# Performance work log

Hardware: AMD Instinct MI355X
Metric: run time of the kernel (lower is better)

## Reference

```python
import jax, jax.numpy as jnp
import numpy as np

DIM = 256
NUM_HEADS = 8
HEAD_DIM = DIM // NUM_HEADS
KERNEL_SIZES = (5, 7, 9)
DILATIONS = (1, 2, 3)
HEADS_PER_RANGE = (4, 3, 1)  # replicates torch allocation: weights~1/k^2, floor + greedy remainder
SCALE = HEAD_DIM ** -0.5


def _unfold(x, ks, dil):
    # x: (B, h, d, H, W) -> (B, h, d, L, H, W), L = ks*ks, same-padded dilated neighborhood gather
    B, h, d, H, W = x.shape
    pad = (ks // 2) * dil
    xp = jnp.pad(x, ((0, 0), (0, 0), (0, 0), (pad, pad), (pad, pad)))
    patches = [xp[..., i * dil:i * dil + H, j * dil:j * dil + W]
               for i in range(ks) for j in range(ks)]
    return jnp.stack(patches, axis=3)


def _attend_range(q, k, v, ks, dil, rpb):
    # q,k,v: (B, h_i, d, H, W); rpb: (h_i, L)
    k_nb = _unfold(k, ks, dil)  # (B,h,d,L,H,W)
    v_nb = _unfold(v, ks, dil)
    logits = jnp.einsum('bhdxy,bhdlxy->bhlxy', q * SCALE, k_nb)
    logits = logits + rpb[None, :, :, None, None]
    attn = jax.nn.softmax(logits, axis=2)
    return jnp.einsum('bhlxy,bhdlxy->bhdxy', attn, v_nb)


def setup_inputs() -> dict:
    key = jax.random.key(0)
    ks = jax.random.split(key, 6)
    B, C, H, W = 4, DIM, 64, 64
    s = 0.02
    inp = {
        'x': jax.random.normal(ks[0], (B, C, H, W), dtype=jnp.float32),
        'qkv_w': jax.random.normal(ks[1], (3 * DIM, DIM), dtype=jnp.float32) * s,
        'qkv_b': jnp.zeros((3 * DIM,), dtype=jnp.float32),
        'proj_w': jax.random.normal(ks[2], (DIM, DIM), dtype=jnp.float32) * s,
        'proj_b': jnp.zeros((DIM,), dtype=jnp.float32),
    }
    for i, kk in enumerate(KERNEL_SIZES):
        inp[f'rpb{i}'] = jax.random.normal(ks[3 + i], (HEADS_PER_RANGE[i], kk * kk), dtype=jnp.float32) * s
    return inp


def reference(x, qkv_w, qkv_b, proj_w, proj_b, rpb0, rpb1, rpb2):
    B, C, H, W = x.shape
    qkv = jnp.einsum('oc,bcxy->boxy', qkv_w, x) + qkv_b[None, :, None, None]
    q, k, v = jnp.split(qkv, 3, axis=1)
    q = q.reshape(B, NUM_HEADS, HEAD_DIM, H, W)
    k = k.reshape(B, NUM_HEADS, HEAD_DIM, H, W)
    v = v.reshape(B, NUM_HEADS, HEAD_DIM, H, W)
    rpbs = (rpb0, rpb1, rpb2)
    outs = []
    hs = 0
    for i in range(len(KERNEL_SIZES)):
        he = hs + HEADS_PER_RANGE[i]
        outs.append(_attend_range(q[:, hs:he], k[:, hs:he], v[:, hs:he],
                                  KERNEL_SIZES[i], DILATIONS[i], rpbs[i]))
        hs = he
    out = jnp.concatenate(outs, axis=1).reshape(B, C, H, W)
    out = jnp.einsum('oc,bcxy->boxy', proj_w, out) + proj_b[None, :, None, None]
    return out
```

## Files before the change

kernel.cpp:

```cpp
#include <hip/hip_runtime.h>
#include <math.h>

#define H_IMG 64
#define W_IMG 64
#define PIX   (H_IMG * W_IMG)
#define NB    4
#define NHEADS 8
#define HD    32
#define CDIM  256
#define QKV_C 768
#define ATT_SCALE 0.17677669529663687f

typedef _Float16 half8_t __attribute__((ext_vector_type(8)));
typedef _Float16 half2_t __attribute__((ext_vector_type(2)));
typedef float f32x4 __attribute__((ext_vector_type(4)));

__global__ void cvt_f16(const float* __restrict__ src, _Float16* __restrict__ dst, int n) {
    int i = blockIdx.x * 256 + threadIdx.x;
    if (i < n) dst[i] = (_Float16)src[i];
}

__launch_bounds__(256)
__global__ void transpose_to_f16(const float* __restrict__ src,
                                 _Float16* __restrict__ dst, int C) {
    __shared__ _Float16 tl[64][66];
    const int b  = blockIdx.z;
    const int p0 = blockIdx.x * 64;
    const int c0 = blockIdx.y * 64;
    const int tx = threadIdx.x;
    const int ty = threadIdx.y;
    const float* s = src + (size_t)b * C * PIX;
    _Float16* d = dst + (size_t)b * PIX * C;
#pragma unroll
    for (int cc = ty; cc < 64; cc += 4)
        tl[cc][tx] = (_Float16)s[(size_t)(c0 + cc) * PIX + p0 + tx];
    __syncthreads();
#pragma unroll
    for (int pp = ty; pp < 64; pp += 4)
        d[(size_t)(p0 + pp) * C + c0 + tx] = tl[tx][pp];
}

template <typename OutT, bool PAIR>
__launch_bounds__(256)
__global__ void gemm16(const _Float16* __restrict__ A,
                       const _Float16* __restrict__ BT,
                       const float* __restrict__ bias,
                       OutT* __restrict__ Y,
                       int M, int K, int N) {
    __shared__ _Float16 Asl[128][40];
    __shared__ _Float16 Bsl[128][40];
    const int b = blockIdx.z;
    const _Float16* Bb = BT + (size_t)b * N * K;
    OutT* Yb = Y + (size_t)b * M * N;
    const int m0 = blockIdx.y * 128;
    const int n0 = blockIdx.x * 128;
    const int t    = threadIdx.x;
    const int lane = t & 63;
    const int w    = t >> 6;
    const int wm = w >> 1, wn = w & 1;
    const int l15 = lane & 15;
    const int kq  = (lane >> 4) * 8;

    f32x4 acc[4][4];
#pragma unroll
    for (int mt = 0; mt < 4; mt++)
#pragma unroll
        for (int nt = 0; nt < 4; nt++)
            acc[mt][nt] = (f32x4){0.f, 0.f, 0.f, 0.f};

    for (int k0 = 0; k0 < K; k0 += 32) {
        __syncthreads();
#pragma unroll
        for (int i = 0; i < 2; i++) {
            int idx = t + i * 256;
            int row = idx >> 2;
            int seg = (idx & 3) * 8;
            *(half8_t*)&Asl[row][seg] = *(const half8_t*)(A  + (size_t)(m0 + row) * K + k0 + seg);
            *(half8_t*)&Bsl[row][seg] = *(const half8_t*)(Bb + (size_t)(n0 + row) * K + k0 + seg);
        }
        __syncthreads();
        half8_t af[4], bf[4];
#pragma unroll
        for (int mt = 0; mt < 4; mt++)
            af[mt] = *(const half8_t*)&Asl[wm * 64 + mt * 16 + l15][kq];
#pragma unroll
        for (int nt = 0; nt < 4; nt++)
            bf[nt] = *(const half8_t*)&Bsl[wn * 64 + nt * 16 + l15][kq];
#pragma unroll
        for (int mt = 0; mt < 4; mt++)
#pragma unroll
            for (int nt = 0; nt < 4; nt++)
                acc[mt][nt] = __builtin_amdgcn_mfma_f32_16x16x32_f16(
                    af[mt], bf[nt], acc[mt][nt], 0, 0, 0);
    }

    const int rq = lane >> 4;
    if constexpr (PAIR) {
        unsigned* Yp = (unsigned*)Yb;
#pragma unroll
        for (int mt = 0; mt < 4; mt++) {
#pragma unroll
            for (int s = 0; s < 2; s++) {
                int mp = m0 + wm * 64 + mt * 16 + rq * 4 + 2 * s;
                float b0 = bias[mp], b1 = bias[mp + 1];
#pragma unroll
                for (int nt = 0; nt < 4; nt++) {
                    int col = n0 + wn * 64 + nt * 16 + l15;
                    half2_t hv;
                    hv.x = (_Float16)(acc[mt][nt][2 * s]     + b0);
                    hv.y = (_Float16)(acc[mt][nt][2 * s + 1] + b1);
                    Yp[(size_t)(mp >> 1) * N + col] = __builtin_bit_cast(unsigned, hv);
                }
            }
        }
    } else {
#pragma unroll
        for (int mt = 0; mt < 4; mt++) {
#pragma unroll
            for (int r = 0; r < 4; r++) {
                int m = m0 + wm * 64 + mt * 16 + rq * 4 + r;
                float bs = bias[m];
                OutT* yp = Yb + (size_t)m * N + n0 + wn * 64;
#pragma unroll
                for (int nt = 0; nt < 4; nt++)
                    yp[nt * 16 + l15] = (OutT)(acc[mt][nt][r] + bs);
            }
        }
    }
}

template <int KS, int DIL>
__device__ __forceinline__ void attn_wave(const unsigned* __restrict__ base,
                                          const float* __restrict__ rp,
                                          float* __restrict__ outp,
                                          int h, int y) {
    const int x = threadIdx.x;

    const unsigned* qb = base + (size_t)(h * 16) * PIX + y * W_IMG + x;
    const unsigned* kb = base + (size_t)(128 + h * 16) * PIX + x;
    const unsigned* vb = base + (size_t)(256 + h * 16) * PIX + x;

    half2_t qh[16];
#pragma unroll
    for (int d2 = 0; d2 < 16; d2++)
        qh[d2] = __builtin_bit_cast(half2_t, qb[(size_t)d2 * PIX]);

    float acc[HD];
#pragma unroll
    for (int d = 0; d < HD; d++) acc[d] = 0.f;
    float denom = 0.f;

#pragma unroll 1
    for (int i = 0; i < KS; i++) {
        const int yy = y + (i - KS / 2) * DIL;
        const float* rrow = rp + i * KS;
        if ((unsigned)yy < (unsigned)H_IMG) {
            int kr[16], vr[16];
            const unsigned* ko = kb + yy * W_IMG;
            const unsigned* vo = vb + yy * W_IMG;
#pragma unroll
            for (int d2 = 0; d2 < 16; d2++) {
                kr[d2] = (int)ko[(size_t)d2 * PIX];
                vr[d2] = (int)vo[(size_t)d2 * PIX];
            }
#pragma unroll
            for (int j = 0; j < KS; j++) {
                const int xx = x + (j - KS / 2) * DIL;
                const int src = xx & 63;
                const bool vx = (unsigned)xx < (unsigned)W_IMG;
                float s = 0.f;
#pragma unroll
                for (int d2 = 0; d2 < 16; d2++) {
                    half2_t kk = __builtin_bit_cast(half2_t, __shfl(kr[d2], src));
#if __has_builtin(__builtin_amdgcn_fdot2)
                    s = __builtin_amdgcn_fdot2(qh[d2], kk, s, false);
#else
                    s += (float)qh[d2].x * (float)kk.x + (float)qh[d2].y * (float)kk.y;
#endif
                }
                const float rb = rrow[j];
                float logit = fmaf(s, ATT_SCALE, rb);
                logit = vx ? logit : rb;
                const float wgt = __expf(logit);
                denom += wgt;
                const float wv = vx ? wgt : 0.f;
#pragma unroll
                for (int d2 = 0; d2 < 16; d2++) {
                    half2_t vv = __builtin_bit_cast(half2_t, __shfl(vr[d2], src));
                    acc[2 * d2]     += wv * (float)vv.x;
                    acc[2 * d2 + 1] += wv * (float)vv.y;
                }
            }
        } else {
#pragma unroll
            for (int j = 0; j < KS; j++) denom += __expf(rrow[j]);
        }
    }

    const float inv = 1.f / denom;
#pragma unroll
    for (int d = 0; d < HD; d++) outp[(size_t)d * PIX] = acc[d] * inv;
}

__launch_bounds__(256)
__global__ void attn_v3(const unsigned* __restrict__ qkv,
                        const float* __restrict__ rpb0,
                        const float* __restrict__ rpb1,
                        const float* __restrict__ rpb2,
                        float* __restrict__ out) {
    const int b  = blockIdx.x >> 1;
    const int hh = blockIdx.x & 1;
    const int y  = blockIdx.y;
    const int ty = threadIdx.y;
    const int h = hh ? (3 + ty) : ((ty == 3) ? 7 : ty);

    const unsigned* base = qkv + (size_t)b * (QKV_C / 2) * PIX;
    float* outp = out + ((size_t)b * CDIM + h * HD) * PIX + y * W_IMG + threadIdx.x;

    if (h < 4) {
        attn_wave<5, 1>(base, rpb0 + h * 25, outp, h, y);
    } else if (h < 7) {
        attn_wave<7, 2>(base, rpb1 + (h - 4) * 49, outp, h, y);
    } else {
        attn_wave<9, 3>(base, rpb2, outp, h, y);
    }
}

extern "C" void kernel_launch(void* const* d_in, const int* in_sizes, int n_in,
                              void* d_out, int out_size, void* d_ws, size_t ws_size,
                              hipStream_t stream) {
    const float* x      = (const float*)d_in[0];
    const float* qkv_w  = (const float*)d_in[1];
    const float* qkv_b  = (const float*)d_in[2];
    const float* proj_w = (const float*)d_in[3];
    const float* proj_b = (const float*)d_in[4];
    const float* rpb0   = (const float*)d_in[5];
    const float* rpb1   = (const float*)d_in[6];
    const float* rpb2   = (const float*)d_in[7];
    float* out = (float*)d_out;

    char* ws = (char*)d_ws;
    _Float16* qkv16 = (_Float16*)ws;
    float*    att32 = (float*)(ws + (size_t)NB * QKV_C * PIX * 2);
    _Float16* T16   = (_Float16*)(ws + (size_t)NB * QKV_C * PIX * 2 + (size_t)NB * CDIM * PIX * 4);
    _Float16* W16   = T16 + (size_t)NB * PIX * CDIM;
    _Float16* P16   = W16 + (size_t)QKV_C * CDIM;

    cvt_f16<<<dim3((QKV_C * CDIM + 255) / 256), dim3(256), 0, stream>>>(qkv_w, W16, QKV_C * CDIM);
    cvt_f16<<<dim3((CDIM * CDIM + 255) / 256), dim3(256), 0, stream>>>(proj_w, P16, CDIM * CDIM);

    transpose_to_f16<<<dim3(PIX / 64, CDIM / 64, NB), dim3(64, 4), 0, stream>>>(x, T16, CDIM);

    gemm16<_Float16, true><<<dim3(PIX / 128, QKV_C / 128, NB), dim3(256), 0, stream>>>(
        W16, T16, qkv_b, qkv16, QKV_C, CDIM, PIX);

    attn_v3<<<dim3(NB * 2, H_IMG), dim3(64, 4), 0, stream>>>(
        (const unsigned*)qkv16, rpb0, rpb1, rpb2, att32);

    transpose_to_f16<<<dim3(PIX / 64, CDIM / 64, NB), dim3(64, 4), 0, stream>>>(att32, T16, CDIM);

    gemm16<float, false><<<dim3(PIX / 128, CDIM / 128, NB), dim3(256), 0, stream>>>(
        P16, T16, proj_b, out, CDIM, CDIM, PIX);
}
```

Before: 171.3 us.

## Fuse attention output transpose into attention kernel and merge weight conversions

The attention kernel now writes fp16 output directly in pixel-major (transposed) layout with 16-byte vector stores. This removes the separate fp32 att buffer and its transpose_to_f16 pass. Blocks are remapped so each block handles one head over four rows, which gives uniform kernel sizes per block instead of mixing heads. The QK dot product is split into four independent accumulators for ILP, and the two weight-conversion launches are merged into one. The strided per-pixel 64-byte stores and rounding the attention output to fp16 before projection are possible costs.

```diff
diff --git a/kernel.cpp b/kernel.cpp
--- a/kernel.cpp
+++ b/kernel.cpp
@@ -15,9 +15,12 @@
 typedef _Float16 half2_t __attribute__((ext_vector_type(2)));
 typedef float f32x4 __attribute__((ext_vector_type(4)));
 
-__global__ void cvt_f16(const float* __restrict__ src, _Float16* __restrict__ dst, int n) {
+__global__ void cvt_w16(const float* __restrict__ a, int na,
+                        const float* __restrict__ b, int nb,
+                        _Float16* __restrict__ da, _Float16* __restrict__ db) {
     int i = blockIdx.x * 256 + threadIdx.x;
-    if (i < n) dst[i] = (_Float16)src[i];
+    if (i < na) da[i] = (_Float16)a[i];
+    else if (i - na < nb) db[i - na] = (_Float16)b[i - na];
 }
 
 __launch_bounds__(256)
@@ -132,7 +135,7 @@
 template <int KS, int DIL>
 __device__ __forceinline__ void attn_wave(const unsigned* __restrict__ base,
                                           const float* __restrict__ rp,
-                                          float* __restrict__ outp,
+                                          _Float16* __restrict__ outp,
                                           int h, int y) {
     const int x = threadIdx.x;
 
@@ -168,18 +171,27 @@
                 const int xx = x + (j - KS / 2) * DIL;
                 const int src = xx & 63;
                 const bool vx = (unsigned)xx < (unsigned)W_IMG;
-                float s = 0.f;
-#pragma unroll
-                for (int d2 = 0; d2 < 16; d2++) {
-                    half2_t kk = __builtin_bit_cast(half2_t, __shfl(kr[d2], src));
+                float s0 = 0.f, s1 = 0.f, s2 = 0.f, s3 = 0.f;
+#pragma unroll
+                for (int d2 = 0; d2 < 16; d2 += 4) {
+                    half2_t k0 = __builtin_bit_cast(half2_t, __shfl(kr[d2 + 0], src));
+                    half2_t k1 = __builtin_bit_cast(half2_t, __shfl(kr[d2 + 1], src));
+                    half2_t k2 = __builtin_bit_cast(half2_t, __shfl(kr[d2 + 2], src));
+                    half2_t k3 = __builtin_bit_cast(half2_t, __shfl(kr[d2 + 3], src));
 #if __has_builtin(__builtin_amdgcn_fdot2)
-                    s = __builtin_amdgcn_fdot2(qh[d2], kk, s, false);
+                    s0 = __builtin_amdgcn_fdot2(qh[d2 + 0], k0, s0, false);
+                    s1 = __builtin_amdgcn_fdot2(qh[d2 + 1], k1, s1, false);
+                    s2 = __builtin_amdgcn_fdot2(qh[d2 + 2], k2, s2, false);
+                    s3 = __builtin_amdgcn_fdot2(qh[d2 + 3], k3, s3, false);
 #else
-                    s += (float)qh[d2].x * (float)kk.x + (float)qh[d2].y * (float)kk.y;
+                    s0 += (float)qh[d2+0].x * (float)k0.x + (float)qh[d2+0].y * (float)k0.y;
+                    s1 += (float)qh[d2+1].x * (float)k1.x + (float)qh[d2+1].y * (float)k1.y;
+                    s2 += (float)qh[d2+2].x * (float)k2.x + (float)qh[d2+2].y * (float)k2.y;
+                    s3 += (float)qh[d2+3].x * (float)k3.x + (float)qh[d2+3].y * (float)k3.y;
 #endif
                 }
                 const float rb = rrow[j];
-                float logit = fmaf(s, ATT_SCALE, rb);
+                float logit = fmaf((s0 + s1) + (s2 + s3), ATT_SCALE, rb);
                 logit = vx ? logit : rb;
                 const float wgt = __expf(logit);
                 denom += wgt;
@@ -199,23 +211,27 @@
 
     const float inv = 1.f / denom;
 #pragma unroll
-    for (int d = 0; d < HD; d++) outp[(size_t)d * PIX] = acc[d] * inv;
+    for (int g = 0; g < 4; g++) {
+        half8_t hv;
+#pragma unroll
+        for (int e = 0; e < 8; e++) hv[e] = (_Float16)(acc[g * 8 + e] * inv);
+        *(half8_t*)(outp + g * 8) = hv;
+    }
 }
 
 __launch_bounds__(256)
-__global__ void attn_v3(const unsigned* __restrict__ qkv,
+__global__ void attn_v4(const unsigned* __restrict__ qkv,
                         const float* __restrict__ rpb0,
                         const float* __restrict__ rpb1,
                         const float* __restrict__ rpb2,
-                        float* __restrict__ out) {
-    const int b  = blockIdx.x >> 1;
-    const int hh = blockIdx.x & 1;
-    const int y  = blockIdx.y;
-    const int ty = threadIdx.y;
-    const int h = hh ? (3 + ty) : ((ty == 3) ? 7 : ty);
+                        _Float16* __restrict__ outT) {
+    const int b = blockIdx.x >> 3;
+    const int h = blockIdx.x & 7;
+    const int y = blockIdx.y * 4 + threadIdx.y;
 
     const unsigned* base = qkv + (size_t)b * (QKV_C / 2) * PIX;
-    float* outp = out + ((size_t)b * CDIM + h * HD) * PIX + y * W_IMG + threadIdx.x;
+    const int p = y * W_IMG + threadIdx.x;
+    _Float16* outp = outT + ((size_t)b * PIX + p) * CDIM + h * HD;
 
     if (h < 4) {
         attn_wave<5, 1>(base, rpb0 + h * 25, outp, h, y);
@@ -241,23 +257,20 @@
 
     char* ws = (char*)d_ws;
     _Float16* qkv16 = (_Float16*)ws;
-    float*    att32 = (float*)(ws + (size_t)NB * QKV_C * PIX * 2);
-    _Float16* T16   = (_Float16*)(ws + (size_t)NB * QKV_C * PIX * 2 + (size_t)NB * CDIM * PIX * 4);
+    _Float16* T16   = (_Float16*)(ws + (size_t)NB * QKV_C * PIX * 2);
     _Float16* W16   = T16 + (size_t)NB * PIX * CDIM;
     _Float16* P16   = W16 + (size_t)QKV_C * CDIM;
 
-    cvt_f16<<<dim3((QKV_C * CDIM + 255) / 256), dim3(256), 0, stream>>>(qkv_w, W16, QKV_C * CDIM);
-    cvt_f16<<<dim3((CDIM * CDIM + 255) / 256), dim3(256), 0, stream>>>(proj_w, P16, CDIM * CDIM);
+    const int nw = QKV_C * CDIM, np = CDIM * CDIM;
+    cvt_w16<<<dim3((nw + np + 255) / 256), dim3(256), 0, stream>>>(qkv_w, nw, proj_w, np, W16, P16);
 
     transpose_to_f16<<<dim3(PIX / 64, CDIM / 64, NB), dim3(64, 4), 0, stream>>>(x, T16, CDIM);
 
     gemm16<_Float16, true><<<dim3(PIX / 128, QKV_C / 128, NB), dim3(256), 0, stream>>>(
         W16, T16, qkv_b, qkv16, QKV_C, CDIM, PIX);
 
-    attn_v3<<<dim3(NB * 2, H_IMG), dim3(64, 4), 0, stream>>>(
-        (const unsigned*)qkv16, rpb0, rpb1, rpb2, att32);
-
-    transpose_to_f16<<<dim3(PIX / 64, CDIM / 64, NB), dim3(64, 4), 0, stream>>>(att32, T16, CDIM);
+    attn_v4<<<dim3(NB * NHEADS, H_IMG / 4), dim3(64, 4), 0, stream>>>(
+        (const unsigned*)qkv16, rpb0, rpb1, rpb2, T16);
 
     gemm16<float, false><<<dim3(PIX / 128, CDIM / 128, NB), dim3(256), 0, stream>>>(
         P16, T16, proj_b, out, CDIM, CDIM, PIX);
```

Result: slower. 176.8 us (+3.2%).
